# Optimization experiments

Measured on AMD Instinct MI355X. Metric: run time of the kernel, lower is better.

Reference implementation:

```python
import jax, jax.numpy as jnp
import numpy as np

DIM = 512
CODEBOOK_SIZE = 8192
B, N = 4, 4096


def setup_inputs() -> dict:
    key = jax.random.key(0)
    k1, k2, k3 = jax.random.split(key, 3)
    scale = DIM ** -0.5
    x = jax.random.normal(k1, (B, N, DIM), dtype=jnp.float32)
    codebook = jax.random.normal(k2, (CODEBOOK_SIZE, DIM), dtype=jnp.float32) * scale
    W = jax.random.normal(k3, (DIM, DIM), dtype=jnp.float32) * scale  # Linear(dim, dim, bias=False) weight
    return {"x": x, "codebook": codebook, "W": W}


def reference(x, codebook, W):
    # implicit_codebook = Linear(codebook): codebook @ W.T   -> [C, D]
    implicit = codebook @ W.T

    # nearest-code search (no grad in original): squared euclidean distance
    x_sg = jax.lax.stop_gradient(x)
    imp_sg = jax.lax.stop_gradient(implicit)
    # [B, N, C] logits; ||x||^2 constant w.r.t. argmin so omitted
    d2 = jnp.sum(imp_sg * imp_sg, axis=-1) - 2.0 * jnp.einsum("bnd,cd->bnc", x_sg, imp_sg)
    indices = jnp.argmin(d2, axis=-1)  # [B, N]

    quantized = implicit[indices]  # gather [B, N, D]

    commit_loss = (
        0.25 * jnp.mean((x - jax.lax.stop_gradient(quantized)) ** 2)
        + jnp.mean((jax.lax.stop_gradient(x) - quantized) ** 2)
    )

    # straight-through estimator
    quantized_st = jax.lax.stop_gradient(quantized - x) + x
    return quantized_st, indices, commit_loss
```

## Files before the change

kernel.cpp:

```cpp
#include <hip/hip_runtime.h>
#include <stdint.h>

#define DIM 512
#define NCODE 8192
#define NTOK 16384
#define QELEMS (NTOK * DIM)
#define IDX_OFF QELEMS
#define LOSS_OFF (QELEMS + NTOK)

#define S_X 21.166666f
#define S_I 423.33334f
#define SXSI 8960.5551f
#define NQ_BIAS 131072
#define MARGIN_INT 3136

#define OFF_NORMS ((size_t)NCODE * DIM * 4)
#define OFF_XI8   (OFF_NORMS + (size_t)NCODE * 4)
#define OFF_II8   (OFF_XI8 + (size_t)NTOK * DIM)
#define OFF_CAND  (OFF_II8 + (size_t)NCODE * DIM)
#define OFF_NQ    (OFF_CAND + (size_t)NTOK * 64 * 4 * 4)

typedef short bf16x8 __attribute__((ext_vector_type(8)));
typedef float f32x4 __attribute__((ext_vector_type(4)));
typedef int   i32x4 __attribute__((ext_vector_type(4)));

__device__ inline unsigned ord32(float f) {
    unsigned u = __float_as_uint(f);
    return (u & 0x80000000u) ? ~u : (u | 0x80000000u);
}
__device__ inline unsigned short f2bf(float f) {
    unsigned u = __float_as_uint(f);
    return (unsigned short)((u + 0x7fffu + ((u >> 16) & 1u)) >> 16);
}
__device__ inline float bf2f(unsigned short h) {
    return __uint_as_float((unsigned)h << 16);
}
__device__ inline int q8(float v, float s) {
    return __float2int_rn(fminf(fmaxf(v * s, -127.f), 127.f));
}
__device__ inline void gl_lds16(const void* g, void* l) {
    __builtin_amdgcn_global_load_lds(
        (const __attribute__((address_space(1))) void*)g,
        (__attribute__((address_space(3))) void*)l, 16, 0, 0);
}

__device__ inline void leaf4(const uint4 v, unsigned r[4]) {
    const unsigned s0 = min(v.x, v.z), t0 = max(v.x, v.z);
    const unsigned s1 = min(v.y, v.w), t1 = max(v.y, v.w);
    r[0] = s0; r[1] = min(t0, s1); r[2] = max(t0, s1); r[3] = t1;
}
__device__ inline void merge44(unsigned a[4], const unsigned b[4]) {
    const unsigned h0 = min(a[0], b[3]), h1 = min(a[1], b[2]);
    const unsigned h2 = min(a[2], b[1]), h3 = min(a[3], b[0]);
    const unsigned l0 = min(h0, h2), u0 = max(h0, h2);
    const unsigned l1 = min(h1, h3), u1 = max(h1, h3);
    a[0] = min(l0, l1); a[1] = max(l0, l1);
    a[2] = min(u0, u1); a[3] = max(u0, u1);
}

__global__ void splitf_kernel(const float* __restrict__ cb,
                              const float* __restrict__ W,
                              unsigned short* __restrict__ cb2,
                              unsigned short* __restrict__ W2,
                              float* __restrict__ norms) {
    const int NCB4 = NCODE * 128;
    int i = blockIdx.x * blockDim.x + threadIdx.x;
    if (i < NCODE) norms[i] = 0.f;
    const float* src;
    unsigned short* dst;
    int k;
    if (i < NCB4) { src = cb; dst = cb2; k = i; }
    else          { src = W;  dst = W2;  k = i - NCB4; }
    float4 v = ((const float4*)src)[k];
    int r = k >> 7;
    int c = (k & 127) << 2;
    unsigned short hx = f2bf(v.x), hy = f2bf(v.y), hz = f2bf(v.z), hw = f2bf(v.w);
    ushort4 hi = {hx, hy, hz, hw};
    ushort4 lo = {f2bf(v.x - bf2f(hx)), f2bf(v.y - bf2f(hy)),
                  f2bf(v.z - bf2f(hz)), f2bf(v.w - bf2f(hw))};
    *(ushort4*)(dst + (size_t)r * 1024 + c) = hi;
    *(ushort4*)(dst + (size_t)r * 1024 + 512 + c) = lo;
}

__global__ __launch_bounds__(256, 2)
void gemm_imp_kernel(const unsigned short* __restrict__ A2,
                     const unsigned short* __restrict__ B2,
                     float* __restrict__ imp, unsigned char* __restrict__ impi8,
                     float* __restrict__ norms) {
    __shared__ __align__(16) unsigned short As2[64 * 64];
    __shared__ __align__(16) unsigned short Bs2[128 * 64];
    const int tid = threadIdx.x;
    const int l = tid & 63;
    const int w = tid >> 6;
    const int row0 = blockIdx.y * 64;
    const int col0 = blockIdx.x * 128;
    const int lr = l & 15;
    const int q = l >> 4;

    const int rr8 = l >> 3;
    const int gch = (l & 7) ^ (rr8 & 7);

    const unsigned short* gA = A2 + (size_t)(row0 + w * 8 + rr8) * 1024 + gch * 8;
    const unsigned short* gB = B2 + (size_t)(col0 + w * 8 + rr8) * 1024 + gch * 8;
    unsigned short* lA = As2 + (w * 8) * 64;
    unsigned short* lB = Bs2 + (w * 8) * 64;

    f32x4 acc[4][2];
    #pragma unroll
    for (int i = 0; i < 4; ++i)
        #pragma unroll
        for (int j = 0; j < 2; ++j) acc[i][j] = (f32x4)0.f;

    for (int c = 0; c < 32; ++c) {
        const int kA = (c & 15) << 6;
        const int kB = (c < 16) ? kA : ((kA + 512) & 1023);
        #pragma unroll
        for (int s = 0; s < 2; ++s)
            gl_lds16(gA + (size_t)(s * 32) * 1024 + kA, lA + (s * 32) * 64);
        #pragma unroll
        for (int s = 0; s < 4; ++s)
            gl_lds16(gB + (size_t)(s * 32) * 1024 + kB, lB + (s * 32) * 64);
        __syncthreads();
        #pragma unroll
        for (int ks = 0; ks < 2; ++ks) {
            const int lc = ks * 4 + q;
            bf16x8 af[4], bf[2];
            #pragma unroll
            for (int i = 0; i < 4; ++i) {
                const int ra = i * 16 + lr;
                af[i] = *(const bf16x8*)(As2 + ra * 64 + ((lc ^ (ra & 7)) << 3));
            }
            #pragma unroll
            for (int j = 0; j < 2; ++j) {
                const int rb = w * 32 + j * 16 + lr;
                bf[j] = *(const bf16x8*)(Bs2 + rb * 64 + ((lc ^ (rb & 7)) << 3));
            }
            #pragma unroll
            for (int i = 0; i < 4; ++i)
                #pragma unroll
                for (int j = 0; j < 2; ++j)
                    acc[i][j] = __builtin_amdgcn_mfma_f32_16x16x32_bf16(
                        af[i], bf[j], acc[i][j], 0, 0, 0);
        }
        __syncthreads();
    }

    #pragma unroll
    for (int i = 0; i < 4; ++i) {
        float np[4] = {0.f, 0.f, 0.f, 0.f};
        #pragma unroll
        for (int j = 0; j < 2; ++j) {
            const int col = col0 + w * 32 + j * 16 + lr;
            #pragma unroll
            for (int r = 0; r < 4; ++r) {
                const int row = row0 + i * 16 + q * 4 + r;
                const float v = acc[i][j][r];
                imp[(size_t)row * DIM + col] = v;
                impi8[(size_t)row * DIM + col] = (unsigned char)(q8(v, S_I) & 0xff);
                np[r] = fmaf(v, v, np[r]);
            }
        }
        #pragma unroll
        for (int r = 0; r < 4; ++r) {
            float s = np[r];
            #pragma unroll
            for (int m = 1; m < 16; m <<= 1) s += __shfl_xor(s, m, 64);
            if (lr == 0)
                atomicAdd(&norms[row0 + i * 16 + q * 4 + r], s);
        }
    }
}

__global__ void cvtx_kernel(const float* __restrict__ src,
                            unsigned char* __restrict__ dst,
                            const float* __restrict__ norms,
                            int* __restrict__ norms_q, int n4) {
    int i = blockIdx.x * blockDim.x + threadIdx.x;
    if (i >= n4) return;
    if (i < NCODE) norms_q[i] = __float2int_rn(norms[i] * SXSI) + NQ_BIAS;
    float4 v = ((const float4*)src)[i];
    unsigned wd = (unsigned)(q8(v.x, S_X) & 0xff)
                | ((unsigned)(q8(v.y, S_X) & 0xff) << 8)
                | ((unsigned)(q8(v.z, S_X) & 0xff) << 16)
                | ((unsigned)(q8(v.w, S_X) & 0xff) << 24);
    ((unsigned*)dst)[i] = wd;
}

__global__ __launch_bounds__(256, 4)
void coarse_kernel(const unsigned char* __restrict__ Xi8,
                   const unsigned char* __restrict__ Ii8,
                   const int* __restrict__ norms_q,
                   unsigned* __restrict__ cand) {
    __shared__ __align__(16) unsigned char smem[32768];
    unsigned* Sw = (unsigned*)smem;

    const int tid = threadIdx.x;
    const int l = tid & 63;
    const int w = tid >> 6;

    const int id = blockIdx.y * 64 + blockIdx.x;
    const int xcd = id & 7;
    const int s8 = id >> 3;
    const int bx = xcd * 8 + (s8 & 7);
    const int by = s8 >> 3;
    const int row0 = by * 128;
    const int col0 = bx * 128;

    const int wm = w & 1, wn = w >> 1;
    const int lr = l & 15;
    const int q = l >> 4;

    const int sl = l >> 3;
    const int eq = (l & 7) ^ sl;
    const int se = eq >> 2;
    const int sq = eq & 3;
    const unsigned char* gA0 =
        Xi8 + (size_t)(row0 + 2 * (w * 8 + sl) + se) * DIM + sq * 16;
    const unsigned char* gB0 =
        Ii8 + (size_t)(col0 + 2 * (w * 8 + sl) + se) * DIM + sq * 16;
    const int ldsA = w * 1024;
    const int ldsB = 8192 + w * 1024;

    const int p8 = ((((lr & 1) << 2) | q) ^ ((lr >> 1) & 7)) << 4;
    const int rdA = (wm * 32 + (lr >> 1)) * 128 + p8;
    const int rdB = 8192 + (wn * 32 + (lr >> 1)) * 128 + p8;

    i32x4 acc[4][4];
    #pragma unroll
    for (int i = 0; i < 4; ++i)
        #pragma unroll
        for (int j = 0; j < 4; ++j) acc[i][j] = (i32x4)0;

#define STAGE(buf, kc) do {                                                  \
        gl_lds16(gA0 + (size_t)(kc),             smem + (buf) + ldsA);       \
        gl_lds16(gA0 + (size_t)64 * DIM + (kc),  smem + (buf) + ldsA + 4096);\
        gl_lds16(gB0 + (size_t)(kc),             smem + (buf) + ldsB);       \
        gl_lds16(gB0 + (size_t)64 * DIM + (kc),  smem + (buf) + ldsB + 4096);\
    } while (0)

    STAGE(0, 0);
    STAGE(16384, 64);

    #pragma unroll
    for (int it = 0; it < 8; ++it) {
        const int cb = (it & 1) * 16384;
        if (it < 7) {
            asm volatile("s_waitcnt vmcnt(4)" ::: "memory");
        } else {
            asm volatile("s_waitcnt vmcnt(0)" ::: "memory");
        }
        __builtin_amdgcn_s_barrier();
        __builtin_amdgcn_sched_barrier(0);
        i32x4 af[4], bfr[4];
        #pragma unroll
        for (int i = 0; i < 4; ++i)
            af[i] = *(const i32x4*)(smem + cb + rdA + i * 1024);
        #pragma unroll
        for (int j = 0; j < 4; ++j)
            bfr[j] = *(const i32x4*)(smem + cb + rdB + j * 1024);
        #pragma unroll
        for (int i = 0; i < 4; ++i)
            #pragma unroll
            for (int j = 0; j < 4; ++j)
                acc[i][j] = __builtin_amdgcn_mfma_i32_16x16x64_i8(
                    af[i], bfr[j], acc[i][j], 0, 0, 0);
        asm volatile("s_waitcnt lgkmcnt(0)" ::: "memory");
        __builtin_amdgcn_sched_barrier(0);
        __builtin_amdgcn_s_barrier();
        if (it < 6) {
            STAGE(cb, (it + 2) << 6);
        }
    }
#undef STAGE

    int nqo[4];
    unsigned codes[4];
    #pragma unroll
    for (int j = 0; j < 4; ++j) {
        codes[j] = (unsigned)(col0 + wn * 64 + j * 16 + lr);
        nqo[j] = norms_q[codes[j]];
    }
    const int c4w = wn * 8 + (lr >> 1);
    const int wsub = (lr & 1) << 1;
    #pragma unroll
    for (int i = 0; i < 4; ++i) {
        #pragma unroll
        for (int r = 0; r < 4; ++r) {
            unsigned pv[4];
            #pragma unroll
            for (int j = 0; j < 4; ++j) {
                int d2o = nqo[j] - 2 * acc[i][j][r];
                d2o = min(max(d2o, 0), 262143);
                pv[j] = ((unsigned)d2o << 13) | codes[j];
            }
            const unsigned s1 = min(pv[0], pv[1]), g1 = max(pv[0], pv[1]);
            const unsigned s2 = min(pv[2], pv[3]), g2 = max(pv[2], pv[3]);
            uint2 o;
            o.x = min(s1, s2);
            o.y = min(max(s1, s2), min(g1, g2));
            const int tok = wm * 64 + i * 16 + q * 4 + r;
            *(uint2*)(Sw + tok * 64 + ((c4w ^ (tok & 7)) << 2) + wsub) = o;
        }
    }
    __syncthreads();

    {
        const int t = tid >> 1, h = tid & 1;
        const unsigned* rowp = Sw + t * 64;
        const int sxor = t & 7;
        unsigned a4[4], b4[4];
        {
            const uint4 va = *(const uint4*)(rowp + (((h * 8 + 0) ^ sxor) << 2));
            const uint4 vb = *(const uint4*)(rowp + (((h * 8 + 1) ^ sxor) << 2));
            leaf4(va, a4); leaf4(vb, b4); merge44(a4, b4);
        }
        #pragma unroll
        for (int p = 1; p < 4; ++p) {
            unsigned c4a[4], c4b[4];
            const uint4 va = *(const uint4*)(rowp + (((h * 8 + 2 * p) ^ sxor) << 2));
            const uint4 vb = *(const uint4*)(rowp + (((h * 8 + 2 * p + 1) ^ sxor) << 2));
            leaf4(va, c4a); leaf4(vb, c4b); merge44(c4a, c4b);
            merge44(a4, c4a);
        }
        const unsigned p3 = (unsigned)__shfl_xor((int)a4[3], 1, 64);
        const unsigned p2 = (unsigned)__shfl_xor((int)a4[2], 1, 64);
        const unsigned u0 = min(a4[0], p3);
        const unsigned u1 = min(a4[1], p2);
        uint2 o2;
        o2.x = h ? u1 : u0;
        o2.y = h ? u0 : u1;
        *(uint2*)(cand + ((size_t)(row0 + t) * 64 + bx) * 4 + h * 2) = o2;
    }
}

__global__ __launch_bounds__(256)
void merge_kernel(const float* __restrict__ X, const float* __restrict__ Imp,
                  const float* __restrict__ norms, const unsigned* __restrict__ cand,
                  float* __restrict__ out, float* __restrict__ lossp) {
    const int t = blockIdx.x * 4 + (threadIdx.x >> 6);
    const int l = threadIdx.x & 63;

    const uint4 c4 = *(const uint4*)(cand + ((size_t)t * 64 + l) * 4);
    unsigned mn = min(min(c4.x, c4.y), min(c4.z, c4.w));
    #pragma unroll
    for (int o = 32; o > 0; o >>= 1)
        mn = min(mn, (unsigned)__shfl_xor((int)mn, o, 64));
    const unsigned th = (mn >> 13) + MARGIN_INT;

    const float4* xp = (const float4*)(X + (size_t)t * DIM);
    const float4 xa = xp[l * 2], xb = xp[l * 2 + 1];

    const unsigned vv[4] = {c4.x, c4.y, c4.z, c4.w};
    unsigned long long best = ~0ull;
    #pragma unroll
    for (int i = 0; i < 4; ++i) {
        const bool pass = (vv[i] >> 13) <= th;
        unsigned long long m = __ballot(pass);
        while (m) {
            const int src = __ffsll((unsigned long long)m) - 1;
            m &= m - 1;
            const int c = __shfl((int)(vv[i] & 8191u), src, 64);
            const float4* ip = (const float4*)(Imp + (size_t)c * DIM);
            const float4 ia = ip[l * 2], ib = ip[l * 2 + 1];
            float s = xa.x * ia.x + xa.y * ia.y + xa.z * ia.z + xa.w * ia.w
                    + xb.x * ib.x + xb.y * ib.y + xb.z * ib.z + xb.w * ib.w;
            #pragma unroll
            for (int o = 32; o > 0; o >>= 1) s += __shfl_xor(s, o, 64);
            const float d = fmaf(-2.f, s, norms[c]);
            const unsigned long long p =
                ((unsigned long long)ord32(d) << 32) | (unsigned)c;
            if (p < best) best = p;
        }
    }
    const int bi = (int)(best & 0xffffffffu);

    const float4* qp = (const float4*)(Imp + (size_t)bi * DIM);
    float4* op = (float4*)(out + (size_t)t * DIM);
    float ls = 0.f;
    #pragma unroll
    for (int jj = 0; jj < 2; ++jj) {
        const int j = l + jj * 64;
        const float4 qv = qp[j], xv = xp[j];
        op[j] = qv;
        const float dx = xv.x - qv.x, dy = xv.y - qv.y,
                    dz = xv.z - qv.z, dw = xv.w - qv.w;
        ls += dx * dx + dy * dy + dz * dz + dw * dw;
    }
    #pragma unroll
    for (int o = 32; o > 0; o >>= 1) ls += __shfl_xor(ls, o, 64);
    if (l == 0) {
        lossp[t] = ls;
        out[IDX_OFF + t] = (float)bi;
    }
}

__global__ __launch_bounds__(1024)
void fin_kernel(const float* __restrict__ lossp, float* __restrict__ out) {
    __shared__ float part[16];
    float s = 0.f;
    for (int i = threadIdx.x; i < NTOK; i += 1024) s += lossp[i];
    #pragma unroll
    for (int o = 32; o > 0; o >>= 1) s += __shfl_xor(s, o, 64);
    if ((threadIdx.x & 63) == 0) part[threadIdx.x >> 6] = s;
    __syncthreads();
    if (threadIdx.x == 0) {
        float tot = 0.f;
        #pragma unroll
        for (int i = 0; i < 16; ++i) tot += part[i];
        out[LOSS_OFF] = 1.25f * tot / (float)QELEMS;
    }
}

extern "C" void kernel_launch(void* const* d_in, const int* in_sizes, int n_in,
                              void* d_out, int out_size, void* d_ws, size_t ws_size,
                              hipStream_t stream) {
    const float* x  = (const float*)d_in[0];
    const float* cb = (const float*)d_in[1];
    const float* W  = (const float*)d_in[2];
    float* out = (float*)d_out;
    char* ws = (char*)d_ws;

    float* imp = (float*)ws;
    float* norms = (float*)(ws + OFF_NORMS);
    unsigned char* xi8 = (unsigned char*)(ws + OFF_XI8);
    unsigned char* ii8 = (unsigned char*)(ws + OFF_II8);
    unsigned* cand = (unsigned*)(ws + OFF_CAND);
    int* norms_q = (int*)(ws + OFF_NQ);
    unsigned short* cb2 = (unsigned short*)(ws + OFF_CAND);
    unsigned short* W2  = (unsigned short*)(ws + OFF_XI8);
    float* lossp = (float*)(ws + OFF_XI8);

    hipLaunchKernelGGL(splitf_kernel, dim3((NCODE * 128 + 512 * 128) / 256),
                       dim3(256), 0, stream, cb, W, cb2, W2, norms);
    hipLaunchKernelGGL(gemm_imp_kernel, dim3(DIM / 128, NCODE / 64), dim3(256), 0,
                       stream, cb2, W2, imp, ii8, norms);
    hipLaunchKernelGGL(cvtx_kernel, dim3(NTOK * DIM / 4 / 256), dim3(256), 0, stream,
                       x, xi8, norms, norms_q, NTOK * DIM / 4);
    hipLaunchKernelGGL(coarse_kernel, dim3(NCODE / 128, NTOK / 128), dim3(256), 0,
                       stream, xi8, ii8, norms_q, cand);
    hipLaunchKernelGGL(merge_kernel, dim3(NTOK / 4), dim3(256), 0, stream,
                       x, imp, norms, cand, out, lossp);
    hipLaunchKernelGGL(fin_kernel, dim3(1), dim3(1024), 0, stream, lossp, out);
}
```

Baseline: 246.2 us.

## Double-buffer implicit-codebook GEMM, pair candidate rescoring, parallelize loss reduction

The implicit-codebook GEMM now uses two LDS buffers with explicit vmcnt waits, so the global-to-LDS loads for step c+2 overlap the MFMA compute on the current step instead of running lock-step with two syncthreads per iteration. The merge kernel rescoring loop handles two candidates per iteration, giving more independent memory loads and shuffle reductions in flight. The final loss reduction is spread over 64 blocks that atomically add into an output zeroed in the first kernel. This doubles LDS use per block, which may reduce occupancy, and the atomic float sum makes the loss order-dependent.

```diff
diff --git a/kernel.cpp b/kernel.cpp
--- a/kernel.cpp
+++ b/kernel.cpp
@@ -62,10 +62,12 @@
                               const float* __restrict__ W,
                               unsigned short* __restrict__ cb2,
                               unsigned short* __restrict__ W2,
-                              float* __restrict__ norms) {
+                              float* __restrict__ norms,
+                              float* __restrict__ out) {
     const int NCB4 = NCODE * 128;
     int i = blockIdx.x * blockDim.x + threadIdx.x;
     if (i < NCODE) norms[i] = 0.f;
+    if (i == 0) out[LOSS_OFF] = 0.f;
     const float* src;
     unsigned short* dst;
     int k;
@@ -87,8 +89,7 @@
                      const unsigned short* __restrict__ B2,
                      float* __restrict__ imp, unsigned char* __restrict__ impi8,
                      float* __restrict__ norms) {
-    __shared__ __align__(16) unsigned short As2[64 * 64];
-    __shared__ __align__(16) unsigned short Bs2[128 * 64];
+    __shared__ __align__(16) unsigned char smem2[49152];
     const int tid = threadIdx.x;
     const int l = tid & 63;
     const int w = tid >> 6;
@@ -102,8 +103,7 @@
 
     const unsigned short* gA = A2 + (size_t)(row0 + w * 8 + rr8) * 1024 + gch * 8;
     const unsigned short* gB = B2 + (size_t)(col0 + w * 8 + rr8) * 1024 + gch * 8;
-    unsigned short* lA = As2 + (w * 8) * 64;
-    unsigned short* lB = Bs2 + (w * 8) * 64;
+    const int wbyte = w * 1024;
 
     f32x4 acc[4][2];
     #pragma unroll
@@ -111,39 +111,73 @@
         #pragma unroll
         for (int j = 0; j < 2; ++j) acc[i][j] = (f32x4)0.f;
 
-    for (int c = 0; c < 32; ++c) {
-        const int kA = (c & 15) << 6;
-        const int kB = (c < 16) ? kA : ((kA + 512) & 1023);
-        #pragma unroll
-        for (int s = 0; s < 2; ++s)
-            gl_lds16(gA + (size_t)(s * 32) * 1024 + kA, lA + (s * 32) * 64);
-        #pragma unroll
-        for (int s = 0; s < 4; ++s)
-            gl_lds16(gB + (size_t)(s * 32) * 1024 + kB, lB + (s * 32) * 64);
-        __syncthreads();
-        #pragma unroll
-        for (int ks = 0; ks < 2; ++ks) {
-            const int lc = ks * 4 + q;
-            bf16x8 af[4], bf[2];
-            #pragma unroll
-            for (int i = 0; i < 4; ++i) {
-                const int ra = i * 16 + lr;
-                af[i] = *(const bf16x8*)(As2 + ra * 64 + ((lc ^ (ra & 7)) << 3));
-            }
-            #pragma unroll
-            for (int j = 0; j < 2; ++j) {
-                const int rb = w * 32 + j * 16 + lr;
-                bf[j] = *(const bf16x8*)(Bs2 + rb * 64 + ((lc ^ (rb & 7)) << 3));
-            }
-            #pragma unroll
-            for (int i = 0; i < 4; ++i)
-                #pragma unroll
-                for (int j = 0; j < 2; ++j)
-                    acc[i][j] = __builtin_amdgcn_mfma_f32_16x16x32_bf16(
-                        af[i], bf[j], acc[i][j], 0, 0, 0);
-        }
-        __syncthreads();
-    }
+#define GSTAGE(bb, kA, kB) do {                                               \
+        gl_lds16(gA + (kA),             smem2 + (bb) + wbyte);                \
+        gl_lds16(gA + 32 * 1024 + (kA), smem2 + (bb) + wbyte + 4096);         \
+        gl_lds16(gB + (kB),             smem2 + (bb) + 8192 + wbyte);         \
+        gl_lds16(gB + 32 * 1024 + (kB), smem2 + (bb) + 8192 + wbyte + 4096);  \
+        gl_lds16(gB + 64 * 1024 + (kB), smem2 + (bb) + 8192 + wbyte + 8192);  \
+        gl_lds16(gB + 96 * 1024 + (kB), smem2 + (bb) + 8192 + wbyte + 12288); \
+    } while (0)
+
+#define GCOMPUTE(bb) do {                                                     \
+        _Pragma("unroll")                                                     \
+        for (int ks = 0; ks < 2; ++ks) {                                      \
+            const int lc = ks * 4 + q;                                        \
+            bf16x8 af[4], bf[2];                                              \
+            _Pragma("unroll")                                                 \
+            for (int i = 0; i < 4; ++i) {                                     \
+                const int ra = i * 16 + lr;                                   \
+                af[i] = *(const bf16x8*)(smem2 + (bb) +                       \
+                         ((ra * 64 + ((lc ^ (ra & 7)) << 3)) << 1));          \
+            }                                                                 \
+            _Pragma("unroll")                                                 \
+            for (int j = 0; j < 2; ++j) {                                     \
+                const int rb = w * 32 + j * 16 + lr;                          \
+                bf[j] = *(const bf16x8*)(smem2 + (bb) + 8192 +                \
+                         ((rb * 64 + ((lc ^ (rb & 7)) << 3)) << 1));          \
+            }                                                                 \
+            _Pragma("unroll")                                                 \
+            for (int i = 0; i < 4; ++i)                                       \
+                _Pragma("unroll")                                             \
+                for (int j = 0; j < 2; ++j)                                   \
+                    acc[i][j] = __builtin_amdgcn_mfma_f32_16x16x32_bf16(      \
+                        af[i], bf[j], acc[i][j], 0, 0, 0);                    \
+        }                                                                     \
+    } while (0)
+
+    GSTAGE(0, 0, 0);
+    GSTAGE(24576, 64, 64);
+
+    for (int c = 0; c < 30; ++c) {
+        const int bb = (c & 1) * 24576;
+        asm volatile("s_waitcnt vmcnt(6)" ::: "memory");
+        __builtin_amdgcn_s_barrier();
+        __builtin_amdgcn_sched_barrier(0);
+        GCOMPUTE(bb);
+        asm volatile("s_waitcnt lgkmcnt(0)" ::: "memory");
+        __builtin_amdgcn_sched_barrier(0);
+        __builtin_amdgcn_s_barrier();
+        {
+            const int c2 = c + 2;
+            const int kA = (c2 & 15) << 6;
+            const int kB = (c2 < 16) ? kA : ((kA + 512) & 1023);
+            GSTAGE(bb, kA, kB);
+        }
+    }
+    asm volatile("s_waitcnt vmcnt(6)" ::: "memory");
+    __builtin_amdgcn_s_barrier();
+    __builtin_amdgcn_sched_barrier(0);
+    GCOMPUTE(0);
+    asm volatile("s_waitcnt lgkmcnt(0)" ::: "memory");
+    __builtin_amdgcn_sched_barrier(0);
+    __builtin_amdgcn_s_barrier();
+    asm volatile("s_waitcnt vmcnt(0)" ::: "memory");
+    __builtin_amdgcn_s_barrier();
+    __builtin_amdgcn_sched_barrier(0);
+    GCOMPUTE(24576);
+#undef GSTAGE
+#undef GCOMPUTE
 
     #pragma unroll
     for (int i = 0; i < 4; ++i) {
@@ -357,19 +391,39 @@
         const bool pass = (vv[i] >> 13) <= th;
         unsigned long long m = __ballot(pass);
         while (m) {
-            const int src = __ffsll((unsigned long long)m) - 1;
+            const int s0i = __ffsll((unsigned long long)m) - 1;
             m &= m - 1;
-            const int c = __shfl((int)(vv[i] & 8191u), src, 64);
-            const float4* ip = (const float4*)(Imp + (size_t)c * DIM);
-            const float4 ia = ip[l * 2], ib = ip[l * 2 + 1];
-            float s = xa.x * ia.x + xa.y * ia.y + xa.z * ia.z + xa.w * ia.w
-                    + xb.x * ib.x + xb.y * ib.y + xb.z * ib.z + xb.w * ib.w;
+            const bool two = (m != 0ull);
+            const int s1i = two ? (__ffsll((unsigned long long)m) - 1) : s0i;
+            if (two) m &= m - 1;
+            const int c0 = __shfl((int)(vv[i] & 8191u), s0i, 64);
+            const int c1 = __shfl((int)(vv[i] & 8191u), s1i, 64);
+            const float4* ip0 = (const float4*)(Imp + (size_t)c0 * DIM);
+            const float4 ia0 = ip0[l * 2], ib0 = ip0[l * 2 + 1];
+            float sb = 0.f;
+            if (two) {
+                const float4* ip1 = (const float4*)(Imp + (size_t)c1 * DIM);
+                const float4 ia1 = ip1[l * 2], ib1 = ip1[l * 2 + 1];
+                sb = xa.x * ia1.x + xa.y * ia1.y + xa.z * ia1.z + xa.w * ia1.w
+                   + xb.x * ib1.x + xb.y * ib1.y + xb.z * ib1.z + xb.w * ib1.w;
+            }
+            float sa = xa.x * ia0.x + xa.y * ia0.y + xa.z * ia0.z + xa.w * ia0.w
+                     + xb.x * ib0.x + xb.y * ib0.y + xb.z * ib0.z + xb.w * ib0.w;
             #pragma unroll
-            for (int o = 32; o > 0; o >>= 1) s += __shfl_xor(s, o, 64);
-            const float d = fmaf(-2.f, s, norms[c]);
-            const unsigned long long p =
-                ((unsigned long long)ord32(d) << 32) | (unsigned)c;
-            if (p < best) best = p;
+            for (int o = 32; o > 0; o >>= 1) {
+                sa += __shfl_xor(sa, o, 64);
+                sb += __shfl_xor(sb, o, 64);
+            }
+            const float d0 = fmaf(-2.f, sa, norms[c0]);
+            const unsigned long long p0 =
+                ((unsigned long long)ord32(d0) << 32) | (unsigned)c0;
+            if (p0 < best) best = p0;
+            if (two) {
+                const float d1 = fmaf(-2.f, sb, norms[c1]);
+                const unsigned long long p1 =
+                    ((unsigned long long)ord32(d1) << 32) | (unsigned)c1;
+                if (p1 < best) best = p1;
+            }
         }
     }
     const int bi = (int)(best & 0xffffffffu);
@@ -394,20 +448,18 @@
     }
 }
 
-__global__ __launch_bounds__(1024)
+__global__ __launch_bounds__(256)
 void fin_kernel(const float* __restrict__ lossp, float* __restrict__ out) {
-    __shared__ float part[16];
-    float s = 0.f;
-    for (int i = threadIdx.x; i < NTOK; i += 1024) s += lossp[i];
+    __shared__ float part[4];
+    const int tid = threadIdx.x;
+    float s = lossp[blockIdx.x * 256 + tid];
     #pragma unroll
     for (int o = 32; o > 0; o >>= 1) s += __shfl_xor(s, o, 64);
-    if ((threadIdx.x & 63) == 0) part[threadIdx.x >> 6] = s;
+    if ((tid & 63) == 0) part[tid >> 6] = s;
     __syncthreads();
-    if (threadIdx.x == 0) {
-        float tot = 0.f;
-        #pragma unroll
-        for (int i = 0; i < 16; ++i) tot += part[i];
-        out[LOSS_OFF] = 1.25f * tot / (float)QELEMS;
+    if (tid == 0) {
+        const float tot = part[0] + part[1] + part[2] + part[3];
+        atomicAdd(&out[LOSS_OFF], 1.25f * tot / (float)QELEMS);
     }
 }
 
@@ -431,7 +483,7 @@
     float* lossp = (float*)(ws + OFF_XI8);
 
     hipLaunchKernelGGL(splitf_kernel, dim3((NCODE * 128 + 512 * 128) / 256),
-                       dim3(256), 0, stream, cb, W, cb2, W2, norms);
+                       dim3(256), 0, stream, cb, W, cb2, W2, norms, out);
     hipLaunchKernelGGL(gemm_imp_kernel, dim3(DIM / 128, NCODE / 64), dim3(256), 0,
                        stream, cb2, W2, imp, ii8, norms);
     hipLaunchKernelGGL(cvtx_kernel, dim3(NTOK * DIM / 4 / 256), dim3(256), 0, stream,
@@ -440,5 +492,5 @@
                        stream, xi8, ii8, norms_q, cand);
     hipLaunchKernelGGL(merge_kernel, dim3(NTOK / 4), dim3(256), 0, stream,
                        x, imp, norms, cand, out, lossp);
-    hipLaunchKernelGGL(fin_kernel, dim3(1), dim3(1024), 0, stream, lossp, out);
-}
+    hipLaunchKernelGGL(fin_kernel, dim3(64), dim3(256), 0, stream, lossp, out);
+}
```

Result: faster. 238.9 us (-3.0%).
